# Kernel optimization log

Hardware: AMD Instinct MI355X
Metric: run time of the kernel (lower is better)

The kernel has to match this reference:

```python
import jax, jax.numpy as jnp
import numpy as np

N, E, B = 16000, 256000, 32
IN, HID, H1, OUT, H2 = 768, 256, 4, 128, 2
LN_EPS = 1e-5


def _gat_layer(x, src, dst, W, a_src, a_dst, b, heads, out, n, concat):
    # x: (n, in), W: (heads*out, in), a_src/a_dst: (heads, out), b: (heads*out,) or (out,)
    h = (x @ W.T).reshape(n, heads, out)                      # (n, H, out)
    alpha_s = (h * a_src).sum(-1)                             # (n, H)
    alpha_d = (h * a_dst).sum(-1)                             # (n, H)
    e = jax.nn.leaky_relu(alpha_s[src] + alpha_d[dst], 0.2)   # (E', H)
    # segment softmax over incoming edges of each dst node
    m = jax.ops.segment_max(e, dst, num_segments=n)           # (n, H)
    ex = jnp.exp(e - m[dst])
    den = jax.ops.segment_sum(ex, dst, num_segments=n)
    alpha = ex / (den[dst] + 1e-16)                           # (E', H)
    msg = h[src] * alpha[..., None]                           # (E', H, out)
    agg = jax.ops.segment_sum(msg, dst, num_segments=n)       # (n, H, out)
    o = agg.reshape(n, heads * out) if concat else agg.mean(axis=1)
    return o + b


def setup_inputs() -> dict:
    key = jax.random.key(0)
    ks = jax.random.split(key, 16)
    x = jax.random.normal(ks[0], (N, IN), dtype=jnp.float32)
    edge_index = jax.random.randint(ks[1], (2, E), 0, N, dtype=jnp.int32)
    batch = jnp.sort(jax.random.randint(ks[2], (N,), 0, B, dtype=jnp.int32))
    s = 0.05
    return {
        "x": x, "edge_index": edge_index, "batch": batch,
        "W1": jax.random.normal(ks[3], (H1 * HID, IN), jnp.float32) * s,
        "a1_src": jax.random.normal(ks[4], (H1, HID), jnp.float32) * s,
        "a1_dst": jax.random.normal(ks[5], (H1, HID), jnp.float32) * s,
        "b1": jnp.zeros((H1 * HID,), jnp.float32),
        "W2": jax.random.normal(ks[6], (H2 * OUT, H1 * HID), jnp.float32) * s,
        "a2_src": jax.random.normal(ks[7], (H2, OUT), jnp.float32) * s,
        "a2_dst": jax.random.normal(ks[8], (H2, OUT), jnp.float32) * s,
        "b2": jnp.zeros((OUT,), jnp.float32),
        "proj_W": jax.random.normal(ks[9], (768, OUT), jnp.float32) * s,
        "proj_b": jnp.zeros((768,), jnp.float32),
        "ln_g": jnp.ones((768,), jnp.float32),
        "ln_b": jnp.zeros((768,), jnp.float32),
    }


def reference(x, edge_index, batch, W1, a1_src, a1_dst, b1,
              W2, a2_src, a2_dst, b2, proj_W, proj_b, ln_g, ln_b):
    # add self-loops (PyG GATConv default add_self_loops=True)
    loop = jnp.arange(N, dtype=edge_index.dtype)
    src = jnp.concatenate([edge_index[0], loop])
    dst = jnp.concatenate([edge_index[1], loop])

    h1 = jax.nn.elu(_gat_layer(x, src, dst, W1, a1_src, a1_dst, b1, H1, HID, N, True))
    # dropout = 0 (eval mode)
    h2 = jax.nn.elu(_gat_layer(h1, src, dst, W2, a2_src, a2_dst, b2, H2, OUT, N, False))

    # global mean pool per graph
    sums = jax.ops.segment_sum(h2, batch, num_segments=B)            # (B, OUT)
    cnt = jax.ops.segment_sum(jnp.ones((N,), h2.dtype), batch, num_segments=B)
    pooled = sums / jnp.maximum(cnt, 1.0)[:, None]

    z = pooled @ proj_W.T + proj_b                                   # (B, 768)
    mu = z.mean(-1, keepdims=True)
    var = ((z - mu) ** 2).mean(-1, keepdims=True)
    graph_embed = (z - mu) / jnp.sqrt(var + LN_EPS) * ln_g + ln_b
    return graph_embed, h2
```

## Files before the change

### kernel.cpp

```cpp
#include <hip/hip_runtime.h>
#include <cstddef>

#define NN   16000
#define NE   256000
#define EP   (NE + NN)
#define BG   32
#define IN_F 768
#define HID  256
#define H1C  4
#define F1   (H1C * HID)
#define OUTF 128
#define H2C  2
#define F2   (H2C * OUTF)

typedef __bf16 bf16x8 __attribute__((ext_vector_type(8)));
typedef float  f32x4  __attribute__((ext_vector_type(4)));
typedef float  f32x2  __attribute__((ext_vector_type(2)));
typedef unsigned short us8 __attribute__((ext_vector_type(8)));

static __device__ __forceinline__ float lrelu02(float x) { return x > 0.f ? x : 0.2f * x; }
static __device__ __forceinline__ float eluf(float x)    { return x > 0.f ? x : expm1f(x); }
static __device__ __forceinline__ unsigned short rne_bf16(float f) {
    unsigned u = __float_as_uint(f);
    return (unsigned short)((u + 0x7fffu + ((u >> 16) & 1u)) >> 16);
}
static __device__ __forceinline__ f32x2 cvt2(unsigned int u) {
    f32x2 r;
    r.x = __uint_as_float(u << 16);
    r.y = __uint_as_float(u & 0xffff0000u);
    return r;
}

#define GLDS16(gp, lp) __builtin_amdgcn_global_load_lds(                         \
    (const __attribute__((address_space(1))) void*)(gp),                          \
    (__attribute__((address_space(3))) void*)(lp), 16, 0, 0)

#define NB_X  ((NN * IN_F) / 1024)
#define NB_W1 ((F1 * IN_F) / 1024)
#define NB_W2 ((F2 * F1) / 1024)
#define NB_H  ((EP + 255) / 256)
#define NB_PREP (NB_X + NB_W1 + NB_W2 + NB_H)

static __device__ __forceinline__ void f2b_body(const float* __restrict__ in,
                                                unsigned short* __restrict__ out,
                                                int blk, int t) {
    int i = (blk * 256 + t) * 4;
    float4 v = *(const float4*)&in[i];
    ushort4 o;
    o.x = rne_bf16(v.x); o.y = rne_bf16(v.y); o.z = rne_bf16(v.z); o.w = rne_bf16(v.w);
    *(ushort4*)&out[i] = o;
}

__global__ __launch_bounds__(256) void k_prep(const float* __restrict__ x,
                                              const float* __restrict__ W1,
                                              const float* __restrict__ W2,
                                              unsigned short* __restrict__ xb,
                                              unsigned short* __restrict__ W1b,
                                              unsigned short* __restrict__ W2b,
                                              const int* __restrict__ ei,
                                              int* __restrict__ deg) {
    int b = blockIdx.x, t = threadIdx.x;
    if (b < NB_X) { f2b_body(x, xb, b, t); return; }
    b -= NB_X;
    if (b < NB_W1) { f2b_body(W1, W1b, b, t); return; }
    b -= NB_W1;
    if (b < NB_W2) { f2b_body(W2, W2b, b, t); return; }
    b -= NB_W2;
    int e = b * 256 + t;
    if (e >= EP) return;
    int d = (e < NE) ? ei[NE + e] : (e - NE);
    atomicAdd(&deg[d], 1);
}

__global__ __launch_bounds__(1024) void k_scan(const int* __restrict__ deg,
                                               int* __restrict__ off, int* __restrict__ cursor) {
    __shared__ int sums[1024];
    int t = threadIdx.x;
    const int CH = 16;
    int base = t * CH;
    int s = 0;
    for (int i = 0; i < CH; ++i) { int idx = base + i; if (idx < NN) s += deg[idx]; }
    sums[t] = s;
    __syncthreads();
    for (int ofs = 1; ofs < 1024; ofs <<= 1) {
        int v = 0;
        if (t >= ofs) v = sums[t - ofs];
        __syncthreads();
        sums[t] += v;
        __syncthreads();
    }
    int run = sums[t] - s;
    for (int i = 0; i < CH; ++i) {
        int idx = base + i;
        if (idx < NN) { off[idx] = run; cursor[idx] = run; run += deg[idx]; }
    }
    if (t == 1023) off[NN] = run;
}

template <int KITER, int HSHIFT, int HCNT>
static __device__ __forceinline__ void gemm_body(const unsigned short* __restrict__ A,
                                                 const unsigned short* __restrict__ B,
                                                 unsigned short* __restrict__ C,
                                                 const float* __restrict__ a_s,
                                                 const float* __restrict__ a_d,
                                                 float* __restrict__ as_o,
                                                 float* __restrict__ ad_o,
                                                 int N, int K, int bx, int by,
                                                 unsigned short* As, unsigned short* Bs,
                                                 int t) {
    const int w = t >> 6, lane = t & 63;
    const int m0 = by * 64, n0 = bx * 128;
    const int wm = (w >> 1) * 32, wn = (w & 1) * 64;

    const unsigned short* ga0 = A + (size_t)(m0 + (t >> 2)) * K + (t & 3) * 8;
    const unsigned short* gb0 = B + (size_t)(n0 + (t >> 2)) * K + (t & 3) * 8;
    const unsigned short* gb1 = gb0 + (size_t)64 * K;
    unsigned short* lA0 = &As[(w * 64) * 8];
    unsigned short* lB0 = &Bs[(w * 64) * 8];
    unsigned short* lB1 = &Bs[(w * 64 + 256) * 8];

    f32x4 acc[2][4] = {};

    const bf16x8* pa = (const bf16x8*)As + (wm + (lane & 15)) * 4 + (lane >> 4);
    const bf16x8* pb = (const bf16x8*)Bs + (wn + (lane & 15)) * 4 + (lane >> 4);

    for (int it = 0; it < KITER; ++it) {
        GLDS16(ga0, lA0);
        GLDS16(gb0, lB0); GLDS16(gb1, lB1);
        ga0 += 32; gb0 += 32; gb1 += 32;
        __syncthreads();
        bf16x8 a0 = pa[0], a1 = pa[64];
        bf16x8 b0 = pb[0], b1 = pb[64], b2 = pb[128], b3 = pb[192];
        acc[0][0] = __builtin_amdgcn_mfma_f32_16x16x32_bf16(a0, b0, acc[0][0], 0, 0, 0);
        acc[0][1] = __builtin_amdgcn_mfma_f32_16x16x32_bf16(a0, b1, acc[0][1], 0, 0, 0);
        acc[0][2] = __builtin_amdgcn_mfma_f32_16x16x32_bf16(a0, b2, acc[0][2], 0, 0, 0);
        acc[0][3] = __builtin_amdgcn_mfma_f32_16x16x32_bf16(a0, b3, acc[0][3], 0, 0, 0);
        acc[1][0] = __builtin_amdgcn_mfma_f32_16x16x32_bf16(a1, b0, acc[1][0], 0, 0, 0);
        acc[1][1] = __builtin_amdgcn_mfma_f32_16x16x32_bf16(a1, b1, acc[1][1], 0, 0, 0);
        acc[1][2] = __builtin_amdgcn_mfma_f32_16x16x32_bf16(a1, b2, acc[1][2], 0, 0, 0);
        acc[1][3] = __builtin_amdgcn_mfma_f32_16x16x32_bf16(a1, b3, acc[1][3], 0, 0, 0);
        __syncthreads();
    }
    const int ccol = n0 + wn + (lane & 15);
    const int crow = m0 + wm + (lane >> 4) * 4;
#pragma unroll
    for (int mi = 0; mi < 2; ++mi)
#pragma unroll
        for (int i = 0; i < 4; ++i) {
            unsigned short* cp = C + (size_t)(crow + mi * 16 + i) * N + ccol;
            cp[0]  = rne_bf16(acc[mi][0][i]);
            cp[16] = rne_bf16(acc[mi][1][i]);
            cp[32] = rne_bf16(acc[mi][2][i]);
            cp[48] = rne_bf16(acc[mi][3][i]);
        }
    const int hh = n0 >> HSHIFT;
    float asv[4], adv[4];
#pragma unroll
    for (int bi = 0; bi < 4; ++bi) {
        asv[bi] = a_s[ccol + bi * 16];
        adv[bi] = a_d[ccol + bi * 16];
    }
#pragma unroll
    for (int mi = 0; mi < 2; ++mi)
#pragma unroll
        for (int i = 0; i < 4; ++i) {
            float vs = acc[mi][0][i] * asv[0] + acc[mi][1][i] * asv[1]
                     + acc[mi][2][i] * asv[2] + acc[mi][3][i] * asv[3];
            float vd = acc[mi][0][i] * adv[0] + acc[mi][1][i] * adv[1]
                     + acc[mi][2][i] * adv[2] + acc[mi][3][i] * adv[3];
#pragma unroll
            for (int m = 1; m <= 8; m <<= 1) {
                vs += __shfl_xor(vs, m);
                vd += __shfl_xor(vd, m);
            }
            if ((lane & 15) == 0) {
                int r = crow + mi * 16 + i;
                atomicAdd(&as_o[r * HCNT + hh], vs);
                atomicAdd(&ad_o[r * HCNT + hh], vd);
            }
        }
}

#define G1_BLKS 2048
__global__ __launch_bounds__(256) void k_gemm1(const unsigned short* __restrict__ A,
                                               const unsigned short* __restrict__ B,
                                               unsigned short* __restrict__ C,
                                               const float* __restrict__ a_s,
                                               const float* __restrict__ a_d,
                                               float* __restrict__ as_o,
                                               float* __restrict__ ad_o,
                                               const int* __restrict__ ei,
                                               int* __restrict__ cursor,
                                               int* __restrict__ csr_src,
                                               int* __restrict__ csr_dst) {
    __shared__ __align__(16) unsigned short As[2048];
    __shared__ __align__(16) unsigned short Bs[4096];
    int blk = blockIdx.x, t = threadIdx.x;
    if (blk < G1_BLKS) {
        int by = (blk & 7) + 8 * (blk >> 6);
        int bx = (blk >> 3) & 7;
        if (by < 250)
            gemm_body<24, 8, 4>(A, B, C, a_s, a_d, as_o, ad_o, F1, IN_F, bx, by, As, Bs, t);
        return;
    }
    int e = (blk - G1_BLKS) * 256 + t;
    if (e >= EP) return;
    int s, d;
    if (e < NE) { s = ei[e]; d = ei[NE + e]; } else { s = d = e - NE; }
    int pos = atomicAdd(&cursor[d], 1);
    csr_src[pos] = s;
    csr_dst[pos] = d;
}

__global__ __launch_bounds__(256) void k_gemm2(const unsigned short* __restrict__ A,
                                               const unsigned short* __restrict__ B,
                                               unsigned short* __restrict__ C,
                                               const float* __restrict__ a_s,
                                               const float* __restrict__ a_d,
                                               float* __restrict__ as_o,
                                               float* __restrict__ ad_o) {
    __shared__ __align__(16) unsigned short As[2048];
    __shared__ __align__(16) unsigned short Bs[4096];
    int blk = blockIdx.x, t = threadIdx.x;
    int by = (blk & 7) + 8 * (blk >> 4);
    int bx = (blk >> 3) & 1;
    if (by < 250)
        gemm_body<32, 7, 2>(A, B, C, a_s, a_d, as_o, ad_o, F2, F1, bx, by, As, Bs, t);
}

__global__ __launch_bounds__(256) void k_el1(const int* __restrict__ csr_src,
                                             const int* __restrict__ csr_dst,
                                             const float* __restrict__ as1,
                                             const float* __restrict__ ad1,
                                             float* __restrict__ el,
                                             float* __restrict__ den) {
    int j = blockIdx.x * 256 + threadIdx.x;
    if (j >= EP) return;
    int s = csr_src[j], d = csr_dst[j];
    float4 av = *(const float4*)&as1[s * H1C];
    float4 dv = *(const float4*)&ad1[d * H1C];
    float4 o;
    o.x = expf(lrelu02(av.x + dv.x));
    o.y = expf(lrelu02(av.y + dv.y));
    o.z = expf(lrelu02(av.z + dv.z));
    o.w = expf(lrelu02(av.w + dv.w));
    *(float4*)&el[(size_t)j * 4] = o;
    atomicAdd(&den[d * H1C + 0], o.x);
    atomicAdd(&den[d * H1C + 1], o.y);
    atomicAdd(&den[d * H1C + 2], o.z);
    atomicAdd(&den[d * H1C + 3], o.w);
}

__global__ __launch_bounds__(256) void k_el2(const int* __restrict__ csr_src,
                                             const int* __restrict__ csr_dst,
                                             const float* __restrict__ as2,
                                             const float* __restrict__ ad2,
                                             float* __restrict__ el) {
    int j = blockIdx.x * 256 + threadIdx.x;
    if (j >= EP) return;
    int s = csr_src[j], d = csr_dst[j];
    float2 av = *(const float2*)&as2[s * 2];
    float2 dv = *(const float2*)&ad2[d * 2];
    float2 o;
    o.x = expf(lrelu02(av.x + dv.x));
    o.y = expf(lrelu02(av.y + dv.y));
    *(float2*)&el[(size_t)j * 2] = o;
}

__global__ __launch_bounds__(256) void k_gat1(const unsigned short* __restrict__ hb,
                                              const float* __restrict__ el,
                                              const float* __restrict__ den,
                                              const int* __restrict__ off,
                                              const int* __restrict__ csr,
                                              const float* __restrict__ b1,
                                              unsigned short* __restrict__ h1b) {
    const int l = threadIdx.x & 63;
    const int w = threadIdx.x >> 6;
    const int s = blockIdx.x & 7;
    const int d = (blockIdx.x >> 3) * 4 + w;
    const int h = s >> 1;
    const int eg = l >> 4;
    const int f0 = s * 128 + (l & 15) * 8;
    const int beg = off[d], end = off[d + 1];
    const float rdh = 1.f / (den[d * H1C + h] + 1e-16f);

    f32x2 acc[4] = {};
    const unsigned int* hbase = (const unsigned int*)hb;
    const int lofs = f0 >> 1;
    for (int cbeg = beg; cbeg < end; cbeg += 64) {
        int cnt = end - cbeg; if (cnt > 64) cnt = 64;
        int idx = cbeg + l;
        int idxc = idx < end ? idx : end - 1;
        int s_sel = csr[idxc];
        float myw = (idx < end) ? el[(size_t)idxc * 4 + h] : 0.f;
        for (int j = 0; j < cnt; j += 4) {
            int src  = __shfl(s_sel, j + eg);
            float wv = __shfl(myw, j + eg);
            uint4 v = *(const uint4*)(hbase + (unsigned)src * (F1 / 2) + lofs);
            f32x2 w2 = {wv, wv};
            acc[0] += w2 * cvt2(v.x); acc[1] += w2 * cvt2(v.y);
            acc[2] += w2 * cvt2(v.z); acc[3] += w2 * cvt2(v.w);
        }
    }
#pragma unroll
    for (int i = 0; i < 4; ++i) {
        acc[i].x += __shfl_xor(acc[i].x, 16);
        acc[i].y += __shfl_xor(acc[i].y, 16);
        acc[i].x += __shfl_xor(acc[i].x, 32);
        acc[i].y += __shfl_xor(acc[i].y, 32);
    }
    if (l < 16) {
        us8 ob;
#pragma unroll
        for (int i = 0; i < 4; ++i) {
            ob[2 * i]     = rne_bf16(eluf(acc[i].x * rdh + b1[f0 + 2 * i]));
            ob[2 * i + 1] = rne_bf16(eluf(acc[i].y * rdh + b1[f0 + 2 * i + 1]));
        }
        *(us8*)&h1b[(size_t)d * F1 + f0] = ob;
    }
}

__global__ __launch_bounds__(256) void k_gat2(const unsigned short* __restrict__ h2b,
                                              const float* __restrict__ el,
                                              const int* __restrict__ off,
                                              const int* __restrict__ csr,
                                              const float* __restrict__ b2,
                                              float* __restrict__ out_h2) {
    const int l = threadIdx.x & 63;
    const int d = blockIdx.x * 4 + (threadIdx.x >> 6);
    const int beg = off[d], end = off[d + 1];
    const int c = l & 31, p = l >> 5;
    const int myhead = c >> 4;
    const int hw = p;

    float s0 = 0.f, s1 = 0.f;
    for (int j = beg + l; j < end; j += 64) {
        float2 e = *(const float2*)&el[(size_t)j * 2];
        s0 += e.x; s1 += e.y;
    }
    for (int o = 32; o > 0; o >>= 1) {
        s0 += __shfl_down(s0, o);
        s1 += __shfl_down(s1, o);
    }
    s0 = __shfl(s0, 0); s1 = __shfl(s1, 0);
    float rdhw = 1.f / ((hw ? s1 : s0) + 1e-16f);

    f32x2 acc[4] = {};
    const unsigned int* base = (const unsigned int*)h2b + c * 4;
    for (int cbeg = beg; cbeg < end; cbeg += 32) {
        int cnt = end - cbeg; if (cnt > 32) cnt = 32;
        int idx = cbeg + c;
        int idxc = idx < end ? idx : end - 1;
        int s_sel = csr[idxc];
        float ev = el[(size_t)idxc * 2 + hw];
        float myw = (idx < end) ? ev * rdhw : 0.f;
        for (int jj = 0; jj < cnt; jj += 8) {
            int e0 = jj + p * 4;
            int sa = __shfl(s_sel, e0 + 0);
            int sb = __shfl(s_sel, e0 + 1);
            int sc = __shfl(s_sel, e0 + 2);
            int sd = __shfl(s_sel, e0 + 3);
            float wa = __shfl(myw, (myhead << 5) | (e0 + 0));
            float wb = __shfl(myw, (myhead << 5) | (e0 + 1));
            float wc = __shfl(myw, (myhead << 5) | (e0 + 2));
            float wd = __shfl(myw, (myhead << 5) | (e0 + 3));
            uint4 va = *(const uint4*)(base + (unsigned)sa * (F2 / 2));
            uint4 vb = *(const uint4*)(base + (unsigned)sb * (F2 / 2));
            uint4 vc = *(const uint4*)(base + (unsigned)sc * (F2 / 2));
            uint4 vd = *(const uint4*)(base + (unsigned)sd * (F2 / 2));
            f32x2 wa2 = {wa, wa}, wb2 = {wb, wb}, wc2 = {wc, wc}, wd2 = {wd, wd};
            acc[0] += wa2 * cvt2(va.x); acc[1] += wa2 * cvt2(va.y);
            acc[2] += wa2 * cvt2(va.z); acc[3] += wa2 * cvt2(va.w);
            acc[0] += wb2 * cvt2(vb.x); acc[1] += wb2 * cvt2(vb.y);
            acc[2] += wb2 * cvt2(vb.z); acc[3] += wb2 * cvt2(vb.w);
            acc[0] += wc2 * cvt2(vc.x); acc[1] += wc2 * cvt2(vc.y);
            acc[2] += wc2 * cvt2(vc.z); acc[3] += wc2 * cvt2(vc.w);
            acc[0] += wd2 * cvt2(vd.x); acc[1] += wd2 * cvt2(vd.y);
            acc[2] += wd2 * cvt2(vd.z); acc[3] += wd2 * cvt2(vd.w);
        }
    }
    float af[8] = {acc[0].x, acc[0].y, acc[1].x, acc[1].y,
                   acc[2].x, acc[2].y, acc[3].x, acc[3].y};
#pragma unroll
    for (int i = 0; i < 8; ++i) af[i] += __shfl(af[i], l ^ 32);
    float pt[8];
#pragma unroll
    for (int i = 0; i < 8; ++i) pt[i] = __shfl(af[i], l ^ 16);
    if (l < 16) {
        int f = l * 8;
        float o[8];
#pragma unroll
        for (int i = 0; i < 8; ++i) o[i] = eluf(0.5f * (af[i] + pt[i]) + b2[f + i]);
        *(float4*)&out_h2[(size_t)d * OUTF + f]     = make_float4(o[0], o[1], o[2], o[3]);
        *(float4*)&out_h2[(size_t)d * OUTF + f + 4] = make_float4(o[4], o[5], o[6], o[7]);
    }
}

__global__ __launch_bounds__(1024) void k_proj_ln(const float* __restrict__ h2,
                                                  const int* __restrict__ batch,
                                                  const float* __restrict__ pW,
                                                  const float* __restrict__ pb,
                                                  const float* __restrict__ g,
                                                  const float* __restrict__ be,
                                                  float* __restrict__ out) {
    __shared__ float part[1024];
    __shared__ float ph[OUTF];
    __shared__ float zb[768];
    __shared__ float red[1024];
    __shared__ float s_mu, s_rstd;
    int b = blockIdx.x, t = threadIdx.x;
    int lo = 0, hi = NN;
    while (lo < hi) { int mid = (lo + hi) >> 1; if (batch[mid] < b) lo = mid + 1; else hi = mid; }
    int n0 = lo;
    lo = 0; hi = NN;
    while (lo < hi) { int mid = (lo + hi) >> 1; if (batch[mid] < b + 1) lo = mid + 1; else hi = mid; }
    int n1 = lo;
    {
        int f = t & 127, slot = t >> 7;
        float a = 0.f;
        for (int n = n0 + slot; n < n1; n += 8) a += h2[(size_t)n * OUTF + f];
        part[t] = a;
    }
    __syncthreads();
    if (t < OUTF) {
        float s = 0.f;
#pragma unroll
        for (int k = 0; k < 8; ++k) s += part[k * 128 + t];
        float c = (float)(n1 - n0);
        c = c < 1.f ? 1.f : c;
        ph[t] = s / c;
    }
    __syncthreads();
    if (t < 768) {
        float acc = pb[t];
        for (int k = 0; k < OUTF; k += 4) {
            float4 w = *(const float4*)&pW[(size_t)t * OUTF + k];
            acc += w.x * ph[k] + w.y * ph[k + 1] + w.z * ph[k + 2] + w.w * ph[k + 3];
        }
        zb[t] = acc;
    }
    __syncthreads();
    red[t] = (t < 768) ? zb[t] : 0.f;
    __syncthreads();
    for (int ofs = 512; ofs > 0; ofs >>= 1) {
        if (t < ofs) red[t] += red[t + ofs];
        __syncthreads();
    }
    if (t == 0) s_mu = red[0] / 768.f;
    __syncthreads();
    float mu = s_mu;
    float dv = (t < 768) ? (zb[t] - mu) : 0.f;
    red[t] = dv * dv;
    __syncthreads();
    for (int ofs = 512; ofs > 0; ofs >>= 1) {
        if (t < ofs) red[t] += red[t + ofs];
        __syncthreads();
    }
    if (t == 0) s_rstd = rsqrtf(red[0] / 768.f + 1e-5f);
    __syncthreads();
    float rstd = s_rstd;
    if (t < 768)
        out[(size_t)b * 768 + t] = (zb[t] - mu) * rstd * g[t] + be[t];
}

extern "C" void kernel_launch(void* const* d_in, const int* in_sizes, int n_in,
                              void* d_out, int out_size, void* d_ws, size_t ws_size,
                              hipStream_t stream) {
    const float* x    = (const float*)d_in[0];
    const int*   ei   = (const int*)d_in[1];
    const int*   batch= (const int*)d_in[2];
    const float* W1   = (const float*)d_in[3];
    const float* a1s  = (const float*)d_in[4];
    const float* a1d  = (const float*)d_in[5];
    const float* b1   = (const float*)d_in[6];
    const float* W2   = (const float*)d_in[7];
    const float* a2s  = (const float*)d_in[8];
    const float* a2d  = (const float*)d_in[9];
    const float* b2   = (const float*)d_in[10];
    const float* pW   = (const float*)d_in[11];
    const float* pb   = (const float*)d_in[12];
    const float* lng  = (const float*)d_in[13];
    const float* lnb  = (const float*)d_in[14];

    float* out_ge = (float*)d_out;
    float* out_h2 = (float*)d_out + BG * 768;

    char* w = (char*)d_ws;
    unsigned short* xb   = (unsigned short*)w;  w += (size_t)NN * IN_F * 2;
    unsigned short* W1b  = (unsigned short*)w;  w += (size_t)F1 * IN_F * 2;
    unsigned short* W2b  = (unsigned short*)w;  w += (size_t)F2 * F1 * 2;
    unsigned short* hbufb= (unsigned short*)w;  w += (size_t)NN * F1 * 2;
    unsigned short* h1b  = (unsigned short*)w;  w += (size_t)NN * F1 * 2;
    unsigned short* h2b  = (unsigned short*)w;  w += (size_t)NN * F2 * 2;
    float* as1  = (float*)w;  w += (size_t)NN * H1C * 4;
    float* ad1  = (float*)w;  w += (size_t)NN * H1C * 4;
    float* as2  = (float*)w;  w += (size_t)NN * H2C * 4;
    float* ad2  = (float*)w;  w += (size_t)NN * H2C * 4;
    float* den1 = (float*)w;  w += (size_t)NN * H1C * 4;
    int* deg    = (int*)w;    w += (size_t)NN * 4;
    int* off    = (int*)w;    w += (size_t)(NN + 4) * 4;
    int* cursor = (int*)w;    w += (size_t)NN * 4;
    int* csr    = (int*)w;    w += (size_t)EP * 4;
    int* csrd   = (int*)w;    w += (size_t)EP * 4;
    float* el1  = (float*)w;  w += (size_t)EP * H1C * 4;
    float* el2  = (float*)w;  w += (size_t)EP * H2C * 4;

    hipMemsetAsync(as1, 0, (size_t)NN * (H1C + H1C + H2C + H2C + H1C + 1) * 4, stream);

    k_prep<<<NB_PREP, 256, 0, stream>>>(x, W1, W2, xb, W1b, W2b, ei, deg);
    k_scan<<<1, 1024, 0, stream>>>(deg, off, cursor);

    k_gemm1<<<G1_BLKS + NB_H, 256, 0, stream>>>(xb, W1b, hbufb, a1s, a1d, as1, ad1,
                                                ei, cursor, csr, csrd);
    k_el1<<<(EP + 255) / 256, 256, 0, stream>>>(csr, csrd, as1, ad1, el1, den1);
    k_gat1<<<(NN / 4) * 8, 256, 0, stream>>>(hbufb, el1, den1, off, csr, b1, h1b);

    k_gemm2<<<512, 256, 0, stream>>>(h1b, W2b, h2b, a2s, a2d, as2, ad2);
    k_el2<<<(EP + 255) / 256, 256, 0, stream>>>(csr, csrd, as2, ad2, el2);
    k_gat2<<<NN / 4, 256, 0, stream>>>(h2b, el2, off, csr, b2, out_h2);

    k_proj_ln<<<BG, 1024, 0, stream>>>(out_h2, batch, pW, pb, lng, lnb, out_ge);
}
```

Baseline: 486.6 us.

## Recast layer-1 GAT aggregation as MFMA over 16-node edge chunks

```diff
diff --git a/kernel.cpp b/kernel.cpp
--- a/kernel.cpp
+++ b/kernel.cpp
@@ -17,6 +17,7 @@
 typedef float  f32x4  __attribute__((ext_vector_type(4)));
 typedef float  f32x2  __attribute__((ext_vector_type(2)));
 typedef unsigned short us8 __attribute__((ext_vector_type(8)));
+typedef unsigned short us4 __attribute__((ext_vector_type(4)));
 
 static __device__ __forceinline__ float lrelu02(float x) { return x > 0.f ? x : 0.2f * x; }
 static __device__ __forceinline__ float eluf(float x)    { return x > 0.f ? x : expm1f(x); }
@@ -232,23 +233,18 @@
                                              const int* __restrict__ csr_dst,
                                              const float* __restrict__ as1,
                                              const float* __restrict__ ad1,
-                                             float* __restrict__ el,
-                                             float* __restrict__ den) {
+                                             unsigned short* __restrict__ el16) {
     int j = blockIdx.x * 256 + threadIdx.x;
     if (j >= EP) return;
     int s = csr_src[j], d = csr_dst[j];
     float4 av = *(const float4*)&as1[s * H1C];
     float4 dv = *(const float4*)&ad1[d * H1C];
-    float4 o;
-    o.x = expf(lrelu02(av.x + dv.x));
-    o.y = expf(lrelu02(av.y + dv.y));
-    o.z = expf(lrelu02(av.z + dv.z));
-    o.w = expf(lrelu02(av.w + dv.w));
-    *(float4*)&el[(size_t)j * 4] = o;
-    atomicAdd(&den[d * H1C + 0], o.x);
-    atomicAdd(&den[d * H1C + 1], o.y);
-    atomicAdd(&den[d * H1C + 2], o.z);
-    atomicAdd(&den[d * H1C + 3], o.w);
+    us4 o;
+    o[0] = rne_bf16(expf(lrelu02(av.x + dv.x)));
+    o[1] = rne_bf16(expf(lrelu02(av.y + dv.y)));
+    o[2] = rne_bf16(expf(lrelu02(av.z + dv.z)));
+    o[3] = rne_bf16(expf(lrelu02(av.w + dv.w)));
+    *(us4*)&el16[(size_t)j * 4] = o;
 }
 
 __global__ __launch_bounds__(256) void k_el2(const int* __restrict__ csr_src,
@@ -268,55 +264,85 @@
 }
 
 __global__ __launch_bounds__(256) void k_gat1(const unsigned short* __restrict__ hb,
-                                              const float* __restrict__ el,
-                                              const float* __restrict__ den,
+                                              const unsigned short* __restrict__ el16,
                                               const int* __restrict__ off,
                                               const int* __restrict__ csr,
+                                              const int* __restrict__ csrd,
                                               const float* __restrict__ b1,
                                               unsigned short* __restrict__ h1b) {
-    const int l = threadIdx.x & 63;
-    const int w = threadIdx.x >> 6;
+    __shared__ __align__(16) char sbuf[4][8192];
+    const int t = threadIdx.x, l = t & 63, w = t >> 6;
     const int s = blockIdx.x & 7;
-    const int d = (blockIdx.x >> 3) * 4 + w;
+    const int db = (blockIdx.x >> 3) * 4 + w;
+    const int d0 = db * 16;
     const int h = s >> 1;
-    const int eg = l >> 4;
-    const int f0 = s * 128 + (l & 15) * 8;
-    const int beg = off[d], end = off[d + 1];
-    const float rdh = 1.f / (den[d * H1C + h] + 1e-16f);
-
-    f32x2 acc[4] = {};
-    const unsigned int* hbase = (const unsigned int*)hb;
-    const int lofs = f0 >> 1;
-    for (int cbeg = beg; cbeg < end; cbeg += 64) {
-        int cnt = end - cbeg; if (cnt > 64) cnt = 64;
-        int idx = cbeg + l;
-        int idxc = idx < end ? idx : end - 1;
-        int s_sel = csr[idxc];
-        float myw = (idx < end) ? el[(size_t)idxc * 4 + h] : 0.f;
-        for (int j = 0; j < cnt; j += 4) {
-            int src  = __shfl(s_sel, j + eg);
-            float wv = __shfl(myw, j + eg);
-            uint4 v = *(const uint4*)(hbase + (unsigned)src * (F1 / 2) + lofs);
-            f32x2 w2 = {wv, wv};
-            acc[0] += w2 * cvt2(v.x); acc[1] += w2 * cvt2(v.y);
-            acc[2] += w2 * cvt2(v.z); acc[3] += w2 * cvt2(v.w);
-        }
-    }
-#pragma unroll
-    for (int i = 0; i < 4; ++i) {
-        acc[i].x += __shfl_xor(acc[i].x, 16);
-        acc[i].y += __shfl_xor(acc[i].y, 16);
-        acc[i].x += __shfl_xor(acc[i].x, 32);
-        acc[i].y += __shfl_xor(acc[i].y, 32);
-    }
-    if (l < 16) {
-        us8 ob;
+    const int g = l >> 4, c = l & 15;
+    const int u = c >> 1, odd = c & 1;
+    const int beg = off[d0], end = off[d0 + 16];
+    char* buf = sbuf[w];
+    const char* rbc = buf + g * 2048 + u * 4 + (odd ? 0 : 32);
+    const unsigned sel = odd ? 0x03020706u : 0x05040100u;
+    const int gfeat = s * 128 + (l >> 3) * 16 + (l & 1) * 8;
+    const int slot_in = (l >> 1) & 3;
+
+    f32x4 acc[8] = {};
+    f32x4 dacc = {};
+    us8 onesu = {0x3F80, 0x3F80, 0x3F80, 0x3F80, 0x3F80, 0x3F80, 0x3F80, 0x3F80};
+    bf16x8 ones = *(bf16x8*)&onesu;
+
+    const int nch = (end - beg + 31) >> 5;
+    for (int ch = 0; ch < nch; ++ch) {
+        const int eb = beg + ch * 32;
+#pragma unroll
+        for (int cc = 0; cc < 8; ++cc) {
+            int slot = eb + cc * 4 + slot_in;
+            int sc = slot < end ? slot : end - 1;
+            int src = csr[sc];
+            GLDS16(hb + (size_t)src * F1 + gfeat, buf + cc * 1024);
+        }
+        us8 au;
+#pragma unroll
+        for (int j = 0; j < 8; ++j) {
+            int slot = eb + g * 8 + j;
+            int sc = slot < end ? slot : end - 1;
+            int dv = csrd[sc];
+            unsigned short ev = el16[(size_t)sc * 4 + h];
+            au[j] = (slot < end && dv == d0 + c) ? ev : (unsigned short)0;
+        }
+        bf16x8 af = *(bf16x8*)&au;
+        asm volatile("s_waitcnt vmcnt(0)" ::: "memory");
+        dacc = __builtin_amdgcn_mfma_f32_16x16x32_bf16(af, ones, dacc, 0, 0, 0);
+#pragma unroll
+        for (int fb = 0; fb < 8; ++fb) {
+            const unsigned* p = (const unsigned*)(rbc + fb * 128);
+            unsigned W0 = p[0], W1 = p[16], W2 = p[256], W3 = p[272];
+            unsigned X0 = (unsigned)__builtin_amdgcn_mov_dpp((int)W0, 0xB1, 0xF, 0xF, true);
+            unsigned X1 = (unsigned)__builtin_amdgcn_mov_dpp((int)W1, 0xB1, 0xF, 0xF, true);
+            unsigned X2 = (unsigned)__builtin_amdgcn_mov_dpp((int)W2, 0xB1, 0xF, 0xF, true);
+            unsigned X3 = (unsigned)__builtin_amdgcn_mov_dpp((int)W3, 0xB1, 0xF, 0xF, true);
+            uint4 qq;
+            qq.x = __builtin_amdgcn_perm(W0, X0, sel);
+            qq.y = __builtin_amdgcn_perm(W1, X1, sel);
+            qq.z = __builtin_amdgcn_perm(W2, X2, sel);
+            qq.w = __builtin_amdgcn_perm(W3, X3, sel);
+            bf16x8 bfv = *(bf16x8*)&qq;
+            acc[fb] = __builtin_amdgcn_mfma_f32_16x16x32_bf16(af, bfv, acc[fb], 0, 0, 0);
+        }
+        asm volatile("s_waitcnt lgkmcnt(0)" ::: "memory");
+    }
+    float rdh[4];
+#pragma unroll
+    for (int i = 0; i < 4; ++i) rdh[i] = 1.f / (dacc[i] + 1e-16f);
+#pragma unroll
+    for (int fb = 0; fb < 8; ++fb) {
+        int f = s * 128 + fb * 16 + c;
+        float bias = b1[f];
 #pragma unroll
         for (int i = 0; i < 4; ++i) {
-            ob[2 * i]     = rne_bf16(eluf(acc[i].x * rdh + b1[f0 + 2 * i]));
-            ob[2 * i + 1] = rne_bf16(eluf(acc[i].y * rdh + b1[f0 + 2 * i + 1]));
-        }
-        *(us8*)&h1b[(size_t)d * F1 + f0] = ob;
+            int r = d0 + g * 4 + i;
+            float v = eluf(acc[fb][i] * rdh[i] + bias);
+            h1b[(size_t)r * F1 + f] = rne_bf16(v);
+        }
     }
 }
 
@@ -496,24 +522,23 @@
     float* ad1  = (float*)w;  w += (size_t)NN * H1C * 4;
     float* as2  = (float*)w;  w += (size_t)NN * H2C * 4;
     float* ad2  = (float*)w;  w += (size_t)NN * H2C * 4;
-    float* den1 = (float*)w;  w += (size_t)NN * H1C * 4;
     int* deg    = (int*)w;    w += (size_t)NN * 4;
     int* off    = (int*)w;    w += (size_t)(NN + 4) * 4;
     int* cursor = (int*)w;    w += (size_t)NN * 4;
     int* csr    = (int*)w;    w += (size_t)EP * 4;
     int* csrd   = (int*)w;    w += (size_t)EP * 4;
-    float* el1  = (float*)w;  w += (size_t)EP * H1C * 4;
+    unsigned short* el16 = (unsigned short*)w;  w += (size_t)EP * H1C * 2;
     float* el2  = (float*)w;  w += (size_t)EP * H2C * 4;
 
-    hipMemsetAsync(as1, 0, (size_t)NN * (H1C + H1C + H2C + H2C + H1C + 1) * 4, stream);
+    hipMemsetAsync(as1, 0, (size_t)NN * (H1C + H1C + H2C + H2C + 1) * 4, stream);
 
     k_prep<<<NB_PREP, 256, 0, stream>>>(x, W1, W2, xb, W1b, W2b, ei, deg);
     k_scan<<<1, 1024, 0, stream>>>(deg, off, cursor);
 
     k_gemm1<<<G1_BLKS + NB_H, 256, 0, stream>>>(xb, W1b, hbufb, a1s, a1d, as1, ad1,
                                                 ei, cursor, csr, csrd);
-    k_el1<<<(EP + 255) / 256, 256, 0, stream>>>(csr, csrd, as1, ad1, el1, den1);
-    k_gat1<<<(NN / 4) * 8, 256, 0, stream>>>(hbufb, el1, den1, off, csr, b1, h1b);
+    k_el1<<<(EP + 255) / 256, 256, 0, stream>>>(csr, csrd, as1, ad1, el16);
+    k_gat1<<<2000, 256, 0, stream>>>(hbufb, el16, off, csr, csrd, b1, h1b);
 
     k_gemm2<<<512, 256, 0, stream>>>(h1b, W2b, h2b, a2s, a2d, as2, ad2);
     k_el2<<<(EP + 255) / 256, 256, 0, stream>>>(csr, csrd, as2, ad2, el2);
```

Result: faster. 413.7 us (-15.0%).
